# Optimization experiments

Hardware: AMD Instinct MI355X
Metric: run time of the kernel (lower is better)

Reference implementation:

```python
import jax, jax.numpy as jnp
import numpy as np

B, N, D = 4, 2048, 1024
H = 16
HD = D // H


def setup_inputs() -> dict:
    key = jax.random.key(0)
    ks = jax.random.split(key, 6)
    x = jax.random.normal(ks[0], (B, N, D), dtype=jnp.float32)
    # additive causal mask: 0 on/below diagonal, -inf above
    neg = jnp.float32(-1e9)
    causal_mask = jnp.where(jnp.triu(jnp.ones((N, N), dtype=bool), k=1), neg, 0.0).astype(jnp.float32)
    s = 1.0 / np.sqrt(D)
    Wqkv = jax.random.normal(ks[1], (D, 3 * D), dtype=jnp.float32) * s
    bqkv = jax.random.normal(ks[2], (3 * D,), dtype=jnp.float32) * 0.01
    Wproj = jax.random.normal(ks[3], (D, D), dtype=jnp.float32) * s
    bproj = jax.random.normal(ks[4], (D,), dtype=jnp.float32) * 0.01
    return {"x": x, "causal_mask": causal_mask, "Wqkv": Wqkv, "bqkv": bqkv, "Wproj": Wproj, "bproj": bproj}


def reference(x, causal_mask, Wqkv, bqkv, Wproj, bproj):
    b, n, d = x.shape
    qkv = x @ Wqkv + bqkv  # [B,N,3D]
    qkv = qkv.reshape(b, n, 3, H, HD).transpose(2, 0, 3, 1, 4)  # [3,B,H,N,HD]
    q, k, v = qkv[0], qkv[1], qkv[2]
    scale = HD ** -0.5
    attn = jnp.einsum('bhqd,bhkd->bhqk', q, k) * scale  # [B,H,N,N]
    attn = attn + causal_mask  # broadcast [N,N] -> [B,H,N,N]
    attn = jax.nn.softmax(attn, axis=-1)
    out = jnp.einsum('bhqk,bhkd->bhqd', attn, v)  # [B,H,N,HD]
    out = out.transpose(0, 2, 1, 3).reshape(b, n, d)
    return out @ Wproj + bproj
```

## Files before the change

kernel.cpp:

```cpp
#include <hip/hip_runtime.h>
#include <hip/hip_bf16.h>

typedef unsigned short u16;
typedef unsigned int u32;
typedef __attribute__((ext_vector_type(8))) short bf16x8;
typedef __attribute__((ext_vector_type(4))) float f32x4;
typedef __attribute__((ext_vector_type(16))) float f32x16;

#define AS1(p) ((const __attribute__((address_space(1))) void*)(p))
#define AS3(p) ((__attribute__((address_space(3))) void*)(p))

#if __has_builtin(__builtin_amdgcn_exp2f)
#define EXP2F(x) __builtin_amdgcn_exp2f(x)
#else
#define EXP2F(x) exp2f(x)
#endif

static __device__ __forceinline__ float b2f(u16 u) {
  union { unsigned int i; float f; } v; v.i = ((unsigned int)u) << 16; return v.f;
}
static __device__ __forceinline__ u16 f2b(float f) {
  union { float f; unsigned int i; } v; v.f = f;
  unsigned int r = v.i + 0x7FFFu + ((v.i >> 16) & 1u);
  return (u16)(r >> 16);
}
static __device__ __forceinline__ u32 cvt_pk_bf16(float lo, float hi) {
  u32 r;
  asm("v_cvt_pk_bf16_f32 %0, %1, %2" : "=v"(r) : "v"(lo), "v"(hi));
  return r;
}
static __device__ __forceinline__ void permswap(u32& a, u32& b) {
  asm("v_permlane32_swap_b32 %0, %1" : "+v"(a), "+v"(b));
}

__global__ __launch_bounds__(256) void cast_f32_bf16(const float* __restrict__ src,
                                                     u16* __restrict__ dst, int n8) {
  int stride = gridDim.x * blockDim.x;
  for (int i = blockIdx.x * blockDim.x + threadIdx.x; i < n8; i += stride) {
    const float4* s = (const float4*)(src + (size_t)i * 8);
    float4 a = s[0], b = s[1];
    bf16x8 o;
    o[0] = (short)f2b(a.x); o[1] = (short)f2b(a.y); o[2] = (short)f2b(a.z); o[3] = (short)f2b(a.w);
    o[4] = (short)f2b(b.x); o[5] = (short)f2b(b.y); o[6] = (short)f2b(b.z); o[7] = (short)f2b(b.w);
    *(bf16x8*)(dst + (size_t)i * 8) = o;
  }
}

__global__ __launch_bounds__(256) void transpose_w(const float* __restrict__ src,
                                                   u16* __restrict__ dst,
                                                   int R, int C) {
  __shared__ float tile[32][33];
  int c0 = blockIdx.x * 32, r0 = blockIdx.y * 32;
  int tx = threadIdx.x, ty = threadIdx.y;
  for (int i = ty; i < 32; i += 8) tile[i][tx] = src[(size_t)(r0 + i) * C + c0 + tx];
  __syncthreads();
  for (int i = ty; i < 32; i += 8) dst[(size_t)(c0 + i) * R + r0 + tx] = f2b(tile[tx][i]);
}

__global__ __launch_bounds__(256) void transpose_v(const u16* __restrict__ qkv,
                                                   u16* __restrict__ VT) {
  const int N = 2048, TD = 3072, D = 1024;
  int bh = blockIdx.y, n0 = blockIdx.x * 64;
  int b = bh >> 4, h = bh & 15;
  int tid = threadIdx.x;
  __shared__ u16 tl[64][72];
  #pragma unroll
  for (int i = 0; i < 16; ++i) {
    int idx = tid + i * 256;
    int nl = idx >> 6, dd = idx & 63;
    tl[dd][nl] = qkv[(size_t)(b * N + n0 + nl) * TD + 2 * D + h * 64 + dd];
  }
  __syncthreads();
  #pragma unroll
  for (int i = 0; i < 16; ++i) {
    int idx = tid + i * 256;
    int dd = idx >> 6, nl = idx & 63;
    VT[((size_t)bh * 64 + dd) * N + n0 + nl] = tl[dd][nl];
  }
}

template <typename OutT>
__global__ __launch_bounds__(256) void gemm_bt_bias(
    const u16* __restrict__ A,
    const u16* __restrict__ BT,
    const float* __restrict__ bias,
    OutT* __restrict__ C,
    int M, int N, int K) {
  __shared__ alignas(16) u16 Als[128 * 32];
  __shared__ alignas(16) u16 Bls[128 * 32];
  const int m0 = blockIdx.x * 128, n0 = blockIdx.y * 128;
  const int t = threadIdx.x;
  const int w = t >> 6, lane = t & 63;
  const int wr = w >> 1, wc = w & 1;
  const int rlo = lane & 15, g = lane >> 4;

  f32x4 acc[4][4] = {};

  const int r0 = t >> 2;
  const int c0 = (t & 3) << 3;
  const u16* aSrc = A + (size_t)(m0 + r0) * K + c0;
  const u16* bSrc = BT + (size_t)(n0 + r0) * K + c0;

  for (int k0 = 0; k0 < K; k0 += 32) {
    __builtin_amdgcn_global_load_lds(AS1(aSrc + k0), AS3(&Als[t * 8]), 16, 0, 0);
    __builtin_amdgcn_global_load_lds(AS1(aSrc + (size_t)64 * K + k0), AS3(&Als[(t + 256) * 8]), 16, 0, 0);
    __builtin_amdgcn_global_load_lds(AS1(bSrc + k0), AS3(&Bls[t * 8]), 16, 0, 0);
    __builtin_amdgcn_global_load_lds(AS1(bSrc + (size_t)64 * K + k0), AS3(&Bls[(t + 256) * 8]), 16, 0, 0);
    __syncthreads();

    bf16x8 a[4], b[4];
    #pragma unroll
    for (int m = 0; m < 4; ++m)
      a[m] = *(const bf16x8*)&Als[(wr * 64 + m * 16 + rlo) * 32 + g * 8];
    #pragma unroll
    for (int n = 0; n < 4; ++n)
      b[n] = *(const bf16x8*)&Bls[(wc * 64 + n * 16 + rlo) * 32 + g * 8];
    #pragma unroll
    for (int m = 0; m < 4; ++m)
      #pragma unroll
      for (int n = 0; n < 4; ++n)
        acc[m][n] = __builtin_amdgcn_mfma_f32_16x16x32_bf16(a[m], b[n], acc[m][n], 0, 0, 0);
    __syncthreads();
  }

  #pragma unroll
  for (int n = 0; n < 4; ++n) {
    const int col = n0 + wc * 64 + n * 16 + rlo;
    const float bv = bias[col];
    #pragma unroll
    for (int m = 0; m < 4; ++m) {
      const int row = m0 + wr * 64 + m * 16 + g * 4;
      #pragma unroll
      for (int i = 0; i < 4; ++i) {
        float r = acc[m][n][i] + bv;
        if constexpr (sizeof(OutT) == 2)
          C[(size_t)(row + i) * N + col] = (OutT)f2b(r);
        else
          C[(size_t)(row + i) * N + col] = (OutT)r;
      }
    }
  }
}

__global__ __launch_bounds__(256) void attn_fwd(
    const u16* __restrict__ qkv,
    const u16* __restrict__ VT,
    u16* __restrict__ O) {
  const int N = 2048, TD = 3072, D = 1024;
  const int bid = blockIdx.x;
  const int qp = bid >> 6, bh = bid & 63;
  const int b = bh >> 4, h = bh & 15;
  const int t = threadIdx.x, w = t >> 6, lane = t & 63;
  const int l31 = lane & 31, hi = lane >> 5;
  const int qbase[2] = {qp * 128 + w * 32, (15 - qp) * 128 + w * 32};

  __shared__ alignas(16) u16 Kls[64 * 64];
  __shared__ alignas(16) u16 Vls[64 * 64];

  bf16x8 qf[2][4];
  #pragma unroll
  for (int m = 0; m < 2; ++m) {
    const u16* qp_ = qkv + ((size_t)(b * N) + qbase[m] + l31) * TD + h * 64 + hi * 8;
    #pragma unroll
    for (int c = 0; c < 4; ++c) {
      bf16x8 v = *(const bf16x8*)(qp_ + c * 16);
      #pragma unroll
      for (int j = 0; j < 8; ++j)
        v[j] = (short)f2b(b2f((u16)v[j]) * 0.125f);
      qf[m][c] = v;
    }
  }

  const int c1 = t, c2 = t + 256;
  const int r1 = c1 >> 3, sc1 = ((c1 & 7) ^ (r1 & 7)) * 8;
  const int r2 = c2 >> 3, sc2 = ((c2 & 7) ^ (r2 & 7)) * 8;
  const u16* kbase = qkv + (size_t)(b * N) * TD + D + h * 64;
  const u16* vbase = VT + (size_t)bh * 64 * N;

  f32x16 o_acc[2][2] = {};
  float psum[2] = {0.f, 0.f};
  const int jend = (15 - qp) * 128 + 64;

  const float L2E = 1.44269504089f;
  const float NSH = -23.0830992f;

  for (int j0 = 0; j0 <= jend; j0 += 64) {
    __builtin_amdgcn_global_load_lds(AS1(kbase + (size_t)(j0 + r1) * TD + sc1), AS3(&Kls[c1 * 8]), 16, 0, 0);
    __builtin_amdgcn_global_load_lds(AS1(kbase + (size_t)(j0 + r2) * TD + sc2), AS3(&Kls[c2 * 8]), 16, 0, 0);
    __builtin_amdgcn_global_load_lds(AS1(vbase + (size_t)r1 * N + j0 + sc1), AS3(&Vls[c1 * 8]), 16, 0, 0);
    __builtin_amdgcn_global_load_lds(AS1(vbase + (size_t)r2 * N + j0 + sc2), AS3(&Vls[c2 * 8]), 16, 0, 0);
    __syncthreads();

    const bool act1 = (j0 <= qbase[1] + 31);
    const bool act0 = (j0 <= qbase[0] + 31);

    if (act1) {
      bf16x8 kf[2][4];
      #pragma unroll
      for (int st = 0; st < 2; ++st) {
        const int row = st * 32 + l31, sw = (row & 7) << 3;
        #pragma unroll
        for (int c = 0; c < 4; ++c)
          kf[st][c] = *(const bf16x8*)&Kls[row * 64 + ((c * 16 + hi * 8) ^ sw)];
      }
      bf16x8 vf[2][2][2];
      #pragma unroll
      for (int dt = 0; dt < 2; ++dt) {
        const int row = dt * 32 + l31, sw = (row & 7) << 3;
        #pragma unroll
        for (int st = 0; st < 2; ++st)
          #pragma unroll
          for (int kc = 0; kc < 2; ++kc)
            vf[st][kc][dt] = *(const bf16x8*)&Vls[row * 64 + ((st * 32 + kc * 16 + hi * 8) ^ sw)];
      }

      #pragma unroll
      for (int m = 0; m < 2; ++m) {
        if (m == 0 && !act0) continue;
        const int qr = qbase[m] + l31;
        const bool straddle = !(j0 + 63 <= qbase[m]);
        #pragma unroll
        for (int st = 0; st < 2; ++st) {
          f32x16 S = {};
          __builtin_amdgcn_s_setprio(1);
          #pragma unroll
          for (int c = 0; c < 4; ++c)
            S = __builtin_amdgcn_mfma_f32_32x32x16_bf16(kf[st][c], qf[m][c], S, 0, 0, 0);
          __builtin_amdgcn_s_setprio(0);
          if (straddle) {
            const int kvb = j0 + st * 32 + 4 * hi;
            #pragma unroll
            for (int r = 0; r < 16; ++r)
              if (kvb + (r & 3) + 8 * (r >> 2) > qr) S[r] = -1e30f;
          }
          float p[16];
          #pragma unroll
          for (int r = 0; r < 16; ++r) p[r] = EXP2F(fmaf(S[r], L2E, NSH));
          float ps = 0.f;
          #pragma unroll
          for (int r = 0; r < 16; ++r) ps += p[r];
          psum[m] += ps;
          u32 wq[8];
          #pragma unroll
          for (int i = 0; i < 8; ++i) wq[i] = cvt_pk_bf16(p[2 * i], p[2 * i + 1]);
          permswap(wq[0], wq[2]); permswap(wq[1], wq[3]);
          permswap(wq[4], wq[6]); permswap(wq[5], wq[7]);
          union { u32 u[4]; bf16x8 v; } pa0, pa1;
          pa0.u[0] = wq[0]; pa0.u[1] = wq[1]; pa0.u[2] = wq[2]; pa0.u[3] = wq[3];
          pa1.u[0] = wq[4]; pa1.u[1] = wq[5]; pa1.u[2] = wq[6]; pa1.u[3] = wq[7];
          __builtin_amdgcn_s_setprio(1);
          #pragma unroll
          for (int dt = 0; dt < 2; ++dt) {
            o_acc[m][dt] = __builtin_amdgcn_mfma_f32_32x32x16_bf16(pa0.v, vf[st][0][dt], o_acc[m][dt], 0, 0, 0);
            o_acc[m][dt] = __builtin_amdgcn_mfma_f32_32x32x16_bf16(pa1.v, vf[st][1][dt], o_acc[m][dt], 0, 0, 0);
          }
          __builtin_amdgcn_s_setprio(0);
        }
      }
    }
    __syncthreads();
  }

  #pragma unroll
  for (int m = 0; m < 2; ++m) {
    float rs = psum[m] + __shfl_xor(psum[m], 32, 64);
    float inv = 1.0f / rs;
    #pragma unroll
    for (int r = 0; r < 16; ++r) {
      const int qrow = (r & 3) + 8 * (r >> 2) + 4 * hi;
      const float invq = __shfl(inv, qrow, 64);
      const int q = qbase[m] + qrow;
      #pragma unroll
      for (int dt = 0; dt < 2; ++dt)
        O[((size_t)(b * N) + q) * D + h * 64 + dt * 32 + l31] = f2b(o_acc[m][dt][r] * invq);
    }
  }
}

extern "C" void kernel_launch(void* const* d_in, const int* in_sizes, int n_in,
                              void* d_out, int out_size, void* d_ws, size_t ws_size,
                              hipStream_t stream) {
  const float* x     = (const float*)d_in[0];
  const float* Wqkv  = (const float*)d_in[2];
  const float* bqkv  = (const float*)d_in[3];
  const float* Wproj = (const float*)d_in[4];
  const float* bproj = (const float*)d_in[5];
  float* out = (float*)d_out;

  const int B = 4, N = 2048, D = 1024, H = 16;
  const int BN = B * N;
  const int TD = 3 * D;

  char* ws = (char*)d_ws;
  u16* qkv    = (u16*)(ws);
  u16* vt     = (u16*)(ws + 50331648);
  u16* aout   = (u16*)(ws + 67108864);
  u16* wqkvT  = (u16*)(ws + 83886080);
  u16* wprojT = (u16*)(ws + 90177536);
  u16* xb     = (u16*)(ws + 92274688);

  cast_f32_bf16<<<2048, 256, 0, stream>>>(x, xb, BN * D / 8);
  transpose_w<<<dim3(TD / 32, D / 32), dim3(32, 8), 0, stream>>>(Wqkv, wqkvT, D, TD);
  transpose_w<<<dim3(D / 32, D / 32), dim3(32, 8), 0, stream>>>(Wproj, wprojT, D, D);
  gemm_bt_bias<u16><<<dim3(BN / 128, TD / 128), 256, 0, stream>>>(xb, wqkvT, bqkv, qkv, BN, TD, D);
  transpose_v<<<dim3(N / 64, B * H), 256, 0, stream>>>(qkv, vt);
  attn_fwd<<<512, 256, 0, stream>>>(qkv, vt, aout);
  gemm_bt_bias<float><<<dim3(BN / 128, D / 128), 256, 0, stream>>>(aout, wprojT, bproj, out, BN, D, D);
}
```

Baseline: 219.1 us.

## Split paired q-tiles into two sequential passes, skipping masked diagonal subtiles

The attention kernel used to handle both paired query tiles (qp and 15-qp) in one sweep over K/V, sharing each K/V LDS tile between them. It now runs two separate passes, one per query tile. This halves the live accumulator and Q-fragment registers, which may raise occupancy, but the K/V tiles for the low tile are loaded twice. It also skips the second 32-key subtile when it lies entirely above the diagonal, removing wasted MFMA and exp work.

```diff
diff --git a/kernel.cpp b/kernel.cpp
--- a/kernel.cpp
+++ b/kernel.cpp
@@ -152,24 +152,9 @@
   const int b = bh >> 4, h = bh & 15;
   const int t = threadIdx.x, w = t >> 6, lane = t & 63;
   const int l31 = lane & 31, hi = lane >> 5;
-  const int qbase[2] = {qp * 128 + w * 32, (15 - qp) * 128 + w * 32};
 
   __shared__ alignas(16) u16 Kls[64 * 64];
   __shared__ alignas(16) u16 Vls[64 * 64];
-
-  bf16x8 qf[2][4];
-  #pragma unroll
-  for (int m = 0; m < 2; ++m) {
-    const u16* qp_ = qkv + ((size_t)(b * N) + qbase[m] + l31) * TD + h * 64 + hi * 8;
-    #pragma unroll
-    for (int c = 0; c < 4; ++c) {
-      bf16x8 v = *(const bf16x8*)(qp_ + c * 16);
-      #pragma unroll
-      for (int j = 0; j < 8; ++j)
-        v[j] = (short)f2b(b2f((u16)v[j]) * 0.125f);
-      qf[m][c] = v;
-    }
-  }
 
   const int c1 = t, c2 = t + 256;
   const int r1 = c1 >> 3, sc1 = ((c1 & 7) ^ (r1 & 7)) * 8;
@@ -177,55 +162,67 @@
   const u16* kbase = qkv + (size_t)(b * N) * TD + D + h * 64;
   const u16* vbase = VT + (size_t)bh * 64 * N;
 
-  f32x16 o_acc[2][2] = {};
-  float psum[2] = {0.f, 0.f};
-  const int jend = (15 - qp) * 128 + 64;
-
   const float L2E = 1.44269504089f;
   const float NSH = -23.0830992f;
 
-  for (int j0 = 0; j0 <= jend; j0 += 64) {
-    __builtin_amdgcn_global_load_lds(AS1(kbase + (size_t)(j0 + r1) * TD + sc1), AS3(&Kls[c1 * 8]), 16, 0, 0);
-    __builtin_amdgcn_global_load_lds(AS1(kbase + (size_t)(j0 + r2) * TD + sc2), AS3(&Kls[c2 * 8]), 16, 0, 0);
-    __builtin_amdgcn_global_load_lds(AS1(vbase + (size_t)r1 * N + j0 + sc1), AS3(&Vls[c1 * 8]), 16, 0, 0);
-    __builtin_amdgcn_global_load_lds(AS1(vbase + (size_t)r2 * N + j0 + sc2), AS3(&Vls[c2 * 8]), 16, 0, 0);
-    __syncthreads();
-
-    const bool act1 = (j0 <= qbase[1] + 31);
-    const bool act0 = (j0 <= qbase[0] + 31);
-
-    if (act1) {
-      bf16x8 kf[2][4];
+  for (int pass = 0; pass < 2; ++pass) {
+    const int qt = pass ? (15 - qp) : qp;
+    const int qbase = qt * 128 + w * 32;
+
+    bf16x8 qf[4];
+    {
+      const u16* qp_ = qkv + ((size_t)(b * N) + qbase + l31) * TD + h * 64 + hi * 8;
       #pragma unroll
-      for (int st = 0; st < 2; ++st) {
-        const int row = st * 32 + l31, sw = (row & 7) << 3;
+      for (int c = 0; c < 4; ++c) {
+        bf16x8 v = *(const bf16x8*)(qp_ + c * 16);
         #pragma unroll
-        for (int c = 0; c < 4; ++c)
-          kf[st][c] = *(const bf16x8*)&Kls[row * 64 + ((c * 16 + hi * 8) ^ sw)];
+        for (int j = 0; j < 8; ++j)
+          v[j] = (short)f2b(b2f((u16)v[j]) * 0.125f);
+        qf[c] = v;
       }
-      bf16x8 vf[2][2][2];
-      #pragma unroll
-      for (int dt = 0; dt < 2; ++dt) {
-        const int row = dt * 32 + l31, sw = (row & 7) << 3;
-        #pragma unroll
-        for (int st = 0; st < 2; ++st)
-          #pragma unroll
-          for (int kc = 0; kc < 2; ++kc)
-            vf[st][kc][dt] = *(const bf16x8*)&Vls[row * 64 + ((st * 32 + kc * 16 + hi * 8) ^ sw)];
-      }
-
-      #pragma unroll
-      for (int m = 0; m < 2; ++m) {
-        if (m == 0 && !act0) continue;
-        const int qr = qbase[m] + l31;
-        const bool straddle = !(j0 + 63 <= qbase[m]);
+    }
+
+    f32x16 o_acc[2] = {};
+    float psum = 0.f;
+    const int jend = qt * 128 + 64;
+
+    for (int j0 = 0; j0 <= jend; j0 += 64) {
+      __builtin_amdgcn_global_load_lds(AS1(kbase + (size_t)(j0 + r1) * TD + sc1), AS3(&Kls[c1 * 8]), 16, 0, 0);
+      __builtin_amdgcn_global_load_lds(AS1(kbase + (size_t)(j0 + r2) * TD + sc2), AS3(&Kls[c2 * 8]), 16, 0, 0);
+      __builtin_amdgcn_global_load_lds(AS1(vbase + (size_t)r1 * N + j0 + sc1), AS3(&Vls[c1 * 8]), 16, 0, 0);
+      __builtin_amdgcn_global_load_lds(AS1(vbase + (size_t)r2 * N + j0 + sc2), AS3(&Vls[c2 * 8]), 16, 0, 0);
+      __syncthreads();
+
+      if (j0 <= qbase + 31) {
+        bf16x8 kf[2][4];
         #pragma unroll
         for (int st = 0; st < 2; ++st) {
+          const int row = st * 32 + l31, sw = (row & 7) << 3;
+          #pragma unroll
+          for (int c = 0; c < 4; ++c)
+            kf[st][c] = *(const bf16x8*)&Kls[row * 64 + ((c * 16 + hi * 8) ^ sw)];
+        }
+        bf16x8 vf[2][2][2];
+        #pragma unroll
+        for (int dt = 0; dt < 2; ++dt) {
+          const int row = dt * 32 + l31, sw = (row & 7) << 3;
+          #pragma unroll
+          for (int st = 0; st < 2; ++st)
+            #pragma unroll
+            for (int kc = 0; kc < 2; ++kc)
+              vf[st][kc][dt] = *(const bf16x8*)&Vls[row * 64 + ((st * 32 + kc * 16 + hi * 8) ^ sw)];
+        }
+
+        const int qr = qbase + l31;
+        const bool straddle = !(j0 + 63 <= qbase);
+        #pragma unroll
+        for (int st = 0; st < 2; ++st) {
+          if (st == 1 && !(j0 < qbase)) continue;
           f32x16 S = {};
           __builtin_amdgcn_s_setprio(1);
           #pragma unroll
           for (int c = 0; c < 4; ++c)
-            S = __builtin_amdgcn_mfma_f32_32x32x16_bf16(kf[st][c], qf[m][c], S, 0, 0, 0);
+            S = __builtin_amdgcn_mfma_f32_32x32x16_bf16(kf[st][c], qf[c], S, 0, 0, 0);
           __builtin_amdgcn_s_setprio(0);
           if (straddle) {
             const int kvb = j0 + st * 32 + 4 * hi;
@@ -239,7 +236,7 @@
           float ps = 0.f;
           #pragma unroll
           for (int r = 0; r < 16; ++r) ps += p[r];
-          psum[m] += ps;
+          psum += ps;
           u32 wq[8];
           #pragma unroll
           for (int i = 0; i < 8; ++i) wq[i] = cvt_pk_bf16(p[2 * i], p[2 * i + 1]);
@@ -251,28 +248,25 @@
           __builtin_amdgcn_s_setprio(1);
           #pragma unroll
           for (int dt = 0; dt < 2; ++dt) {
-            o_acc[m][dt] = __builtin_amdgcn_mfma_f32_32x32x16_bf16(pa0.v, vf[st][0][dt], o_acc[m][dt], 0, 0, 0);
-            o_acc[m][dt] = __builtin_amdgcn_mfma_f32_32x32x16_bf16(pa1.v, vf[st][1][dt], o_acc[m][dt], 0, 0, 0);
+            o_acc[dt] = __builtin_amdgcn_mfma_f32_32x32x16_bf16(pa0.v, vf[st][0][dt], o_acc[dt], 0, 0, 0);
+            o_acc[dt] = __builtin_amdgcn_mfma_f32_32x32x16_bf16(pa1.v, vf[st][1][dt], o_acc[dt], 0, 0, 0);
           }
           __builtin_amdgcn_s_setprio(0);
         }
       }
+      __syncthreads();
     }
-    __syncthreads();
-  }
-
-  #pragma unroll
-  for (int m = 0; m < 2; ++m) {
-    float rs = psum[m] + __shfl_xor(psum[m], 32, 64);
+
+    float rs = psum + __shfl_xor(psum, 32, 64);
     float inv = 1.0f / rs;
     #pragma unroll
     for (int r = 0; r < 16; ++r) {
       const int qrow = (r & 3) + 8 * (r >> 2) + 4 * hi;
       const float invq = __shfl(inv, qrow, 64);
-      const int q = qbase[m] + qrow;
+      const int q = qbase + qrow;
       #pragma unroll
       for (int dt = 0; dt < 2; ++dt)
-        O[((size_t)(b * N) + q) * D + h * 64 + dt * 32 + l31] = f2b(o_acc[m][dt][r] * invq);
+        O[((size_t)(b * N) + q) * D + h * 64 + dt * 32 + l31] = f2b(o_acc[dt][r] * invq);
     }
   }
 }
```

New measurement: 194.5 us. -11.3%, faster.
